# Performance work log

Hardware: AMD Instinct MI355X
Metric: run time of the kernel (lower is better)

The kernel has to match this reference:

```python
import jax, jax.numpy as jnp
import numpy as np

N_NODES = 100000
N_EDGES = 3200000
N_FEAT = 256
N_CLASS = 40
K_HOPS = 2


def setup_inputs() -> dict:
    key = jax.random.key(0)
    k1, k2, k3, k4, k5 = jax.random.split(key, 5)
    x = jax.random.normal(k1, (N_NODES, N_FEAT), dtype=jnp.float32)
    edge_index = jax.random.randint(k2, (2, N_EDGES), 0, N_NODES, dtype=jnp.int64)
    edge_weight = jax.random.uniform(k3, (N_EDGES,), dtype=jnp.float32)
    W = jax.random.normal(k4, (N_CLASS, N_FEAT), dtype=jnp.float32) / np.sqrt(N_FEAT)
    b = jax.random.normal(k5, (N_CLASS,), dtype=jnp.float32) * 0.01
    return {"x": x, "edge_index": edge_index, "edge_weight": edge_weight, "W": W, "b": b}


def _sgc_forward(x, edge_index, edge_weight, W, b):
    n = x.shape[0]
    # gcn_norm with add_self_loops=True (SGConv default, fill_value=1.0)
    self_idx = jnp.arange(n, dtype=edge_index.dtype)
    row = jnp.concatenate([edge_index[0], self_idx])
    col = jnp.concatenate([edge_index[1], self_idx])
    w = jnp.concatenate([edge_weight, jnp.ones((n,), dtype=edge_weight.dtype)])
    deg = jax.ops.segment_sum(w, col, num_segments=n)  # degree at targets
    dinv = jnp.where(deg > 0, jax.lax.rsqrt(deg), 0.0)
    norm = dinv[row] * w * dinv[col]  # [E+N]
    # K-hop propagation: out[col] += norm * x[row]
    for _ in range(K_HOPS):
        x = jax.ops.segment_sum(norm[:, None] * x[row], col, num_segments=n)
    logits = x @ W.T + b  # [N, nclass]
    return jax.nn.log_softmax(logits, axis=1)


def reference(x, edge_index, edge_weight, W, b):
    return _sgc_forward(x, edge_index, edge_weight, W, b)
```

## Files before the change

kernel.cpp:

```cpp
#include <hip/hip_runtime.h>
#include <hip/hip_fp16.h>
#include <cmath>

#define NNODES 100000
#define NEDGES 3200000
#define NFEAT 256
#define NCLASS 40

#define BSHIFT 8
#define BSIZE 256
#define NBUCK ((NNODES + BSIZE - 1) / BSIZE)
#define CAP 9216
#define ECHUNK 8192
#define CSTH 512
#define EPT (ECHUNK / CSTH)
#define NCB ((NEDGES + ECHUNK - 1) / ECHUNK)
#define EPTF (CAP / 512)


using bf16x8 = __attribute__((ext_vector_type(8))) short;
using f32x4 = __attribute__((ext_vector_type(4))) float;

__device__ inline unsigned pk2(float a, float b) {
    __half2 h;
    h.x = __float2half_rn(a);
    h.y = __float2half_rn(b);
    return *reinterpret_cast<unsigned*>(&h);
}
__device__ inline float2 up2(unsigned u) {
    __half2 h = *reinterpret_cast<__half2*>(&u);
    float2 f;
    f.x = __half2float(h.x);
    f.y = __half2float(h.y);
    return f;
}
__device__ inline unsigned short f2bf(float f) {
    unsigned u = __float_as_uint(f);
    unsigned r = (u + 0x7FFFu + ((u >> 16) & 1u)) >> 16;
    return (unsigned short)r;
}

__global__ void detect_kernel(const int* __restrict__ eidx, int* __restrict__ flag) {
    __shared__ int odd_nz;
    if (threadIdx.x == 0) odd_nz = 0;
    __syncthreads();
    int local = 0;
    for (int i = threadIdx.x; i < 2048; i += blockDim.x) {
        if (eidx[2 * i + 1] != 0) local = 1;
    }
    if (local) atomicOr(&odd_nz, 1);
    __syncthreads();
    if (threadIdx.x == 0) *flag = odd_nz ? 1 : 2;
}

__global__ void __launch_bounds__(CSTH) cscatter_kernel(const int* __restrict__ eidx,
                                                        const float* __restrict__ ew,
                                                        int2* __restrict__ coarse,
                                                        int* __restrict__ cursor,
                                                        const int* __restrict__ flag) {
    __shared__ int h[NBUCK];
    __shared__ int lbase[NBUCK];
    int t = threadIdx.x;
    for (int i = t; i < NBUCK; i += CSTH) h[i] = 0;
    __syncthreads();
    int stride = *flag;
    long long cb = (long long)NEDGES * stride;
    int e0 = blockIdx.x * ECHUNK;
    int bk[EPT];
    int pk[EPT];
    float wv[EPT];
#pragma unroll
    for (int i = 0; i < EPT; i++) {
        int e = e0 + t + i * CSTH;
        if (e < NEDGES) {
            int col = eidx[cb + (long long)e * stride];
            int src = eidx[(long long)e * stride];
            wv[i] = ew[e];
            bk[i] = col >> BSHIFT;
            pk[i] = (src << BSHIFT) | (col & (BSIZE - 1));
            atomicAdd(&h[bk[i]], 1);
        } else {
            bk[i] = -1;
        }
    }
    __syncthreads();
    for (int i = t; i < NBUCK; i += CSTH) {
        int c = h[i];
        lbase[i] = c ? atomicAdd(&cursor[i], c) : 0;
        h[i] = 0;
    }
    __syncthreads();
#pragma unroll
    for (int i = 0; i < EPT; i++) {
        if (bk[i] >= 0) {
            int pos = lbase[bk[i]] + atomicAdd(&h[bk[i]], 1);
            coarse[(size_t)bk[i] * CAP + pos] = make_int2(pk[i], __float_as_int(wv[i]));
        }
    }
}

__global__ void __launch_bounds__(512) fine_kernel(int2* __restrict__ coarse,
                                                   const int* __restrict__ cursor,
                                                   int* __restrict__ rowptr,
                                                   int* __restrict__ rowend,
                                                   float* __restrict__ dinv,
                                                   const int* __restrict__ unused) {
    __shared__ int hist[BSIZE];
    __shared__ float wdeg[BSIZE];
    __shared__ int foff[BSIZE];
    __shared__ int sa[BSIZE], sb[BSIZE];
    int t = threadIdx.x;
    int bk = blockIdx.x;
    size_t base = (size_t)bk * CAP;
    if (t < BSIZE) { hist[t] = 0; wdeg[t] = 0.f; }
    __syncthreads();
    int cnt = cursor[bk];
    int2 st[EPTF];
#pragma unroll
    for (int i = 0; i < EPTF; i++) {
        int idx = t + i * 512;
        if (idx < cnt) st[i] = coarse[base + idx];
    }
#pragma unroll
    for (int i = 0; i < EPTF; i++) {
        int idx = t + i * 512;
        if (idx < cnt) {
            int loc = st[i].x & (BSIZE - 1);
            atomicAdd(&hist[loc], 1);
            atomicAdd(&wdeg[loc], __int_as_float(st[i].y));
        }
    }
    __syncthreads();
    int gcol = (bk << BSHIFT) + t;
    if (t < BSIZE) {
        float dv = rsqrtf(wdeg[t] + 1.0f);
        if (gcol < NNODES) dinv[gcol] = dv;
        sa[t] = hist[t];
    }
    __syncthreads();
    int* s = sa; int* d = sb;
    for (int off = 1; off < BSIZE; off <<= 1) {
        if (t < BSIZE) d[t] = s[t] + ((t >= off) ? s[t - off] : 0);
        __syncthreads();
        int* tmp = s; s = d; d = tmp;
    }
    if (t < BSIZE) {
        foff[t] = (t == 0) ? 0 : s[t - 1];
        hist[t] = 0;
        if (gcol < NNODES) {
            rowptr[gcol] = (int)base + foff[t];
            rowend[gcol] = (int)base + s[t];
        }
    }
    __syncthreads();
#pragma unroll
    for (int i = 0; i < EPTF; i++) {
        int idx = t + i * 512;
        if (idx < cnt) {
            int loc = st[i].x & (BSIZE - 1);
            int srcn = ((unsigned)st[i].x) >> BSHIFT;
            int pos = foff[loc] + atomicAdd(&hist[loc], 1);
            coarse[base + pos] = make_int2(srcn, st[i].y);
        }
    }
}

__global__ void wconv_kernel(const float* __restrict__ W, unsigned short* __restrict__ wt) {
    int i = blockIdx.x * 256 + threadIdx.x;
    if (i >= 48 * 256) return;
    int n = i >> 8;
    wt[i] = (n < NCLASS) ? f2bf(W[i]) : (unsigned short)0;
}

__global__ void __launch_bounds__(256) gemm_mfma_kernel(const float* __restrict__ x,
                                                        const unsigned short* __restrict__ wt,
                                                        const float* __restrict__ dinv,
                                                        __half* __restrict__ y0h) {
    int wv = threadIdx.x >> 6;
    int lane = threadIdx.x & 63;
    int r = lane & 15;
    int kg = lane >> 4;
    int mbase = blockIdx.x * 64 + wv * 16;
    int anode = mbase + r;
    bool aok = anode < NNODES;
    const float* ap = x + (size_t)anode * NFEAT + kg * 8;

    f32x4 acc0 = {0.f, 0.f, 0.f, 0.f};
    f32x4 acc1 = {0.f, 0.f, 0.f, 0.f};
    f32x4 acc2 = {0.f, 0.f, 0.f, 0.f};
#pragma unroll
    for (int ks = 0; ks < 8; ks++) {
        int k0 = ks * 32 + kg * 8;
        bf16x8 af;
        if (aok) {
            float4 p0 = *(const float4*)(ap + ks * 32);
            float4 p1 = *(const float4*)(ap + ks * 32 + 4);
            af[0] = (short)f2bf(p0.x); af[1] = (short)f2bf(p0.y);
            af[2] = (short)f2bf(p0.z); af[3] = (short)f2bf(p0.w);
            af[4] = (short)f2bf(p1.x); af[5] = (short)f2bf(p1.y);
            af[6] = (short)f2bf(p1.z); af[7] = (short)f2bf(p1.w);
        } else {
            af = bf16x8{0, 0, 0, 0, 0, 0, 0, 0};
        }
        bf16x8 b0 = *(const bf16x8*)(wt + (0 * 16 + r) * NFEAT + k0);
        bf16x8 b1 = *(const bf16x8*)(wt + (1 * 16 + r) * NFEAT + k0);
        bf16x8 b2 = *(const bf16x8*)(wt + (2 * 16 + r) * NFEAT + k0);
        acc0 = __builtin_amdgcn_mfma_f32_16x16x32_bf16(af, b0, acc0, 0, 0, 0);
        acc1 = __builtin_amdgcn_mfma_f32_16x16x32_bf16(af, b1, acc1, 0, 0, 0);
        acc2 = __builtin_amdgcn_mfma_f32_16x16x32_bf16(af, b2, acc2, 0, 0, 0);
    }
#pragma unroll
    for (int j = 0; j < 4; j++) {
        int node = mbase + kg * 4 + j;
        if (node >= NNODES) continue;
        float dv = dinv[node];
        __half* yr = y0h + (size_t)node * 64;
        yr[r] = __float2half_rn(acc0[j] * dv);
        yr[16 + r] = __float2half_rn(acc1[j] * dv);
        if (r < 8) yr[32 + r] = __float2half_rn(acc2[j] * dv);
    }
}

__global__ void __launch_bounds__(320) hop16_kernel(const int* __restrict__ rowptr,
                                                    const int* __restrict__ rowend,
                                                    const int2* __restrict__ csr,
                                                    const float* __restrict__ dinv,
                                                    const uint4* __restrict__ yin,
                                                    uint4* __restrict__ yout) {
    int tid = threadIdx.x;
    int ln = tid / 5;
    int c = tid - ln * 5;
    int n = blockIdx.x * 64 + ln;
    if (n >= NNODES) return;
    float d = dinv[n];
    float dd = d * d;
    uint4 sv = yin[(size_t)n * 8 + c];
    float a0, a1, a2, a3, a4, a5, a6, a7;
    { float2 u0 = up2(sv.x), u1 = up2(sv.y), u2 = up2(sv.z), u3 = up2(sv.w);
      a0 = u0.x; a1 = u0.y; a2 = u1.x; a3 = u1.y; a4 = u2.x; a5 = u2.y; a6 = u3.x; a7 = u3.y; }
    int e0 = rowptr[n], e1 = rowend[n];
    int e = e0;
    for (; e + 8 <= e1; e += 8) {
        int2 p[8];
        uint4 g[8];
#pragma unroll
        for (int i = 0; i < 8; i++) p[i] = csr[e + i];
#pragma unroll
        for (int i = 0; i < 8; i++) g[i] = yin[(size_t)p[i].x * 8 + c];
#pragma unroll
        for (int i = 0; i < 8; i++) {
            float w = __int_as_float(p[i].y);
            float2 u0 = up2(g[i].x), u1 = up2(g[i].y), u2 = up2(g[i].z), u3 = up2(g[i].w);
            a0 += w * u0.x; a1 += w * u0.y; a2 += w * u1.x; a3 += w * u1.y;
            a4 += w * u2.x; a5 += w * u2.y; a6 += w * u3.x; a7 += w * u3.y;
        }
    }
    for (; e < e1; e++) {
        int2 p = csr[e];
        uint4 g = yin[(size_t)p.x * 8 + c];
        float w = __int_as_float(p.y);
        float2 u0 = up2(g.x), u1 = up2(g.y), u2 = up2(g.z), u3 = up2(g.w);
        a0 += w * u0.x; a1 += w * u0.y; a2 += w * u1.x; a3 += w * u1.y;
        a4 += w * u2.x; a5 += w * u2.y; a6 += w * u3.x; a7 += w * u3.y;
    }
    uint4 o;
    o.x = pk2(dd * a0, dd * a1); o.y = pk2(dd * a2, dd * a3);
    o.z = pk2(dd * a4, dd * a5); o.w = pk2(dd * a6, dd * a7);
    yout[(size_t)n * 8 + c] = o;
}

__global__ void __launch_bounds__(320) hop32_kernel(const int* __restrict__ rowptr,
                                                    const int* __restrict__ rowend,
                                                    const int2* __restrict__ csr,
                                                    const float* __restrict__ dinv,
                                                    const uint4* __restrict__ yin,
                                                    const float* __restrict__ bias,
                                                    float* __restrict__ out) {
    __shared__ float redm[64][5];
    __shared__ float reds[64][5];
    int tid = threadIdx.x;
    int ln = tid / 5;
    int c = tid - ln * 5;
    int n = blockIdx.x * 64 + ln;
    bool alive = n < NNODES;
    float d = alive ? dinv[n] : 0.f;
    float a0 = 0, a1 = 0, a2 = 0, a3 = 0, a4 = 0, a5 = 0, a6 = 0, a7 = 0;
    int e0 = 0, e1 = 0;
    if (alive) {
        uint4 sv = yin[(size_t)n * 8 + c];
        float2 u0 = up2(sv.x), u1 = up2(sv.y), u2 = up2(sv.z), u3 = up2(sv.w);
        a0 = u0.x; a1 = u0.y; a2 = u1.x; a3 = u1.y; a4 = u2.x; a5 = u2.y; a6 = u3.x; a7 = u3.y;
        e0 = rowptr[n]; e1 = rowend[n];
    }
    int e = e0;
    for (; e + 8 <= e1; e += 8) {
        int2 p[8];
        uint4 g[8];
#pragma unroll
        for (int i = 0; i < 8; i++) p[i] = csr[e + i];
#pragma unroll
        for (int i = 0; i < 8; i++) g[i] = yin[(size_t)p[i].x * 8 + c];
#pragma unroll
        for (int i = 0; i < 8; i++) {
            float w = __int_as_float(p[i].y);
            float2 u0 = up2(g[i].x), u1 = up2(g[i].y), u2 = up2(g[i].z), u3 = up2(g[i].w);
            a0 += w * u0.x; a1 += w * u0.y; a2 += w * u1.x; a3 += w * u1.y;
            a4 += w * u2.x; a5 += w * u2.y; a6 += w * u3.x; a7 += w * u3.y;
        }
    }
    for (; e < e1; e++) {
        int2 p = csr[e];
        uint4 g = yin[(size_t)p.x * 8 + c];
        float w = __int_as_float(p.y);
        float2 u0 = up2(g.x), u1 = up2(g.y), u2 = up2(g.z), u3 = up2(g.w);
        a0 += w * u0.x; a1 += w * u0.y; a2 += w * u1.x; a3 += w * u1.y;
        a4 += w * u2.x; a5 += w * u2.y; a6 += w * u3.x; a7 += w * u3.y;
    }
    float4 b0 = *(const float4*)(bias + c * 8);
    float4 b1 = *(const float4*)(bias + c * 8 + 4);
    float v0 = d * a0 + b0.x, v1 = d * a1 + b0.y, v2 = d * a2 + b0.z, v3 = d * a3 + b0.w;
    float v4 = d * a4 + b1.x, v5 = d * a5 + b1.y, v6 = d * a6 + b1.z, v7 = d * a7 + b1.w;
    float mm = fmaxf(fmaxf(fmaxf(v0, v1), fmaxf(v2, v3)), fmaxf(fmaxf(v4, v5), fmaxf(v6, v7)));
    redm[ln][c] = mm;
    __syncthreads();
    if (c == 0) {
        float m = redm[ln][0];
#pragma unroll
        for (int j = 1; j < 5; j++) m = fmaxf(m, redm[ln][j]);
        redm[ln][0] = m;
    }
    __syncthreads();
    float m = redm[ln][0];
    float ss = __expf(v0 - m) + __expf(v1 - m) + __expf(v2 - m) + __expf(v3 - m)
             + __expf(v4 - m) + __expf(v5 - m) + __expf(v6 - m) + __expf(v7 - m);
    reds[ln][c] = ss;
    __syncthreads();
    if (c == 0) {
        float s = 0.f;
#pragma unroll
        for (int j = 0; j < 5; j++) s += reds[ln][j];
        reds[ln][0] = logf(s);
    }
    __syncthreads();
    float ls = reds[ln][0];
    if (alive) {
        float* op = out + (size_t)n * NCLASS + c * 8;
        *(float4*)op = make_float4(v0 - m - ls, v1 - m - ls, v2 - m - ls, v3 - m - ls);
        *(float4*)(op + 4) = make_float4(v4 - m - ls, v5 - m - ls, v6 - m - ls, v7 - m - ls);
    }
}

extern "C" void kernel_launch(void* const* d_in, const int* in_sizes, int n_in,
                              void* d_out, int out_size, void* d_ws, size_t ws_size,
                              hipStream_t stream) {
    const float* x = (const float*)d_in[0];
    const int* eidx = (const int*)d_in[1];
    const float* ew = (const float*)d_in[2];
    const float* W = (const float*)d_in[3];
    const float* b = (const float*)d_in[4];
    float* out = (float*)d_out;

    char* ws = (char*)d_ws;
    size_t off = 0;
    auto alloc = [&](size_t bytes) -> char* {
        char* p = ws + off;
        off += (bytes + 255) & ~(size_t)255;
        return p;
    };
    int* flag = (int*)alloc(sizeof(int));
    int* cursor = (int*)alloc((size_t)NBUCK * 4);
    int* rowptr = (int*)alloc((size_t)NNODES * 4);
    int* rowend = (int*)alloc((size_t)NNODES * 4);
    float* dinv = (float*)alloc((size_t)NNODES * 4);
    unsigned short* wt = (unsigned short*)alloc((size_t)48 * 256 * 2);
    int2* gcsr = (int2*)alloc((size_t)NBUCK * CAP * 8);
    __half* y0h = (__half*)alloc((size_t)NNODES * 128);
    __half* y1h = (__half*)alloc((size_t)NNODES * 128);

    hipMemsetAsync(cursor, 0, (size_t)NBUCK * 4, stream);
    detect_kernel<<<1, 256, 0, stream>>>(eidx, flag);
    wconv_kernel<<<48, 256, 0, stream>>>(W, wt);
    cscatter_kernel<<<NCB, CSTH, 0, stream>>>(eidx, ew, gcsr, cursor, flag);
    fine_kernel<<<NBUCK, 512, 0, stream>>>(gcsr, cursor, rowptr, rowend, dinv, flag);
    gemm_mfma_kernel<<<(NNODES + 63) / 64, 256, 0, stream>>>(x, wt, dinv, y0h);
    hop16_kernel<<<(NNODES + 63) / 64, 320, 0, stream>>>(rowptr, rowend, gcsr, dinv,
                                                         (const uint4*)y0h, (uint4*)y1h);
    hop32_kernel<<<(NNODES + 63) / 64, 320, 0, stream>>>(rowptr, rowend, gcsr, dinv,
                                                         (const uint4*)y1h, b, out);
}
```

Before: 248.9 us.

## Split propagation into column slabs and pack CSR entries into 32 bits

Splits the 40-class feature matrix into three narrow slabs (16, 16, 8 columns) that are each propagated through both hops separately, so each slab's gather working set is smaller and more cache-resident. CSR entries are packed into 32 bits (17-bit source index plus a 15-bit half-precision weight), halving index traffic, and row start and end are merged into one int2. Log-softmax moves to a separate wave-reduction kernel that re-reads the logits. The cost is three times the CSR traversals, more launches, an extra pass over the output, and reduced weight precision.

```diff
diff --git a/kernel.cpp b/kernel.cpp
--- a/kernel.cpp
+++ b/kernel.cpp
@@ -101,10 +101,8 @@
 
 __global__ void __launch_bounds__(512) fine_kernel(int2* __restrict__ coarse,
                                                    const int* __restrict__ cursor,
-                                                   int* __restrict__ rowptr,
-                                                   int* __restrict__ rowend,
-                                                   float* __restrict__ dinv,
-                                                   const int* __restrict__ unused) {
+                                                   int2* __restrict__ rowmeta,
+                                                   float* __restrict__ dinv) {
     __shared__ int hist[BSIZE];
     __shared__ float wdeg[BSIZE];
     __shared__ int foff[BSIZE];
@@ -112,6 +110,8 @@
     int t = threadIdx.x;
     int bk = blockIdx.x;
     size_t base = (size_t)bk * CAP;
+    unsigned* csr32 = (unsigned*)coarse;
+    int base2 = bk * CAP * 2;
     if (t < BSIZE) { hist[t] = 0; wdeg[t] = 0.f; }
     __syncthreads();
     int cnt = cursor[bk];
@@ -147,10 +147,7 @@
     if (t < BSIZE) {
         foff[t] = (t == 0) ? 0 : s[t - 1];
         hist[t] = 0;
-        if (gcol < NNODES) {
-            rowptr[gcol] = (int)base + foff[t];
-            rowend[gcol] = (int)base + s[t];
-        }
+        if (gcol < NNODES) rowmeta[gcol] = make_int2(base2 + foff[t], base2 + s[t]);
     }
     __syncthreads();
 #pragma unroll
@@ -158,9 +155,10 @@
         int idx = t + i * 512;
         if (idx < cnt) {
             int loc = st[i].x & (BSIZE - 1);
-            int srcn = ((unsigned)st[i].x) >> BSHIFT;
+            unsigned srcn = ((unsigned)st[i].x) >> BSHIFT;
             int pos = foff[loc] + atomicAdd(&hist[loc], 1);
-            coarse[base + pos] = make_int2(srcn, st[i].y);
+            unsigned wb = (unsigned)__half_as_ushort(__float2half_rn(__int_as_float(st[i].y))) & 0x7FFFu;
+            csr32[base2 + pos] = (srcn << 15) | wb;
         }
     }
 }
@@ -175,7 +173,9 @@
 __global__ void __launch_bounds__(256) gemm_mfma_kernel(const float* __restrict__ x,
                                                         const unsigned short* __restrict__ wt,
                                                         const float* __restrict__ dinv,
-                                                        __half* __restrict__ y0h) {
+                                                        __half* __restrict__ S0,
+                                                        __half* __restrict__ S1,
+                                                        __half* __restrict__ S2) {
     int wv = threadIdx.x >> 6;
     int lane = threadIdx.x & 63;
     int r = lane & 15;
@@ -214,51 +214,49 @@
         int node = mbase + kg * 4 + j;
         if (node >= NNODES) continue;
         float dv = dinv[node];
-        __half* yr = y0h + (size_t)node * 64;
-        yr[r] = __float2half_rn(acc0[j] * dv);
-        yr[16 + r] = __float2half_rn(acc1[j] * dv);
-        if (r < 8) yr[32 + r] = __float2half_rn(acc2[j] * dv);
-    }
-}
-
-__global__ void __launch_bounds__(320) hop16_kernel(const int* __restrict__ rowptr,
-                                                    const int* __restrict__ rowend,
-                                                    const int2* __restrict__ csr,
-                                                    const float* __restrict__ dinv,
-                                                    const uint4* __restrict__ yin,
-                                                    uint4* __restrict__ yout) {
-    int tid = threadIdx.x;
-    int ln = tid / 5;
-    int c = tid - ln * 5;
-    int n = blockIdx.x * 64 + ln;
+        S0[(size_t)node * 16 + r] = __float2half_rn(acc0[j] * dv);
+        S1[(size_t)node * 16 + r] = __float2half_rn(acc1[j] * dv);
+        if (r < 8) S2[(size_t)node * 8 + r] = __float2half_rn(acc2[j] * dv);
+    }
+}
+
+template <int LPN>
+__global__ void __launch_bounds__(320) hopA_kernel(const int2* __restrict__ rowmeta,
+                                                   const unsigned* __restrict__ csr,
+                                                   const float* __restrict__ dinv,
+                                                   const uint4* __restrict__ yin,
+                                                   uint4* __restrict__ yout) {
+    int idx = blockIdx.x * blockDim.x + threadIdx.x;
+    int n = idx / LPN;
+    int half = idx - n * LPN;
     if (n >= NNODES) return;
     float d = dinv[n];
     float dd = d * d;
-    uint4 sv = yin[(size_t)n * 8 + c];
+    int2 rm = rowmeta[n];
+    uint4 sv = yin[(size_t)n * LPN + half];
     float a0, a1, a2, a3, a4, a5, a6, a7;
     { float2 u0 = up2(sv.x), u1 = up2(sv.y), u2 = up2(sv.z), u3 = up2(sv.w);
       a0 = u0.x; a1 = u0.y; a2 = u1.x; a3 = u1.y; a4 = u2.x; a5 = u2.y; a6 = u3.x; a7 = u3.y; }
-    int e0 = rowptr[n], e1 = rowend[n];
-    int e = e0;
+    int e = rm.x, e1 = rm.y;
     for (; e + 8 <= e1; e += 8) {
-        int2 p[8];
+        unsigned p[8];
         uint4 g[8];
 #pragma unroll
         for (int i = 0; i < 8; i++) p[i] = csr[e + i];
 #pragma unroll
-        for (int i = 0; i < 8; i++) g[i] = yin[(size_t)p[i].x * 8 + c];
+        for (int i = 0; i < 8; i++) g[i] = yin[(size_t)(p[i] >> 15) * LPN + half];
 #pragma unroll
         for (int i = 0; i < 8; i++) {
-            float w = __int_as_float(p[i].y);
+            float w = __half2float(__ushort_as_half((unsigned short)(p[i] & 0x7FFFu)));
             float2 u0 = up2(g[i].x), u1 = up2(g[i].y), u2 = up2(g[i].z), u3 = up2(g[i].w);
             a0 += w * u0.x; a1 += w * u0.y; a2 += w * u1.x; a3 += w * u1.y;
             a4 += w * u2.x; a5 += w * u2.y; a6 += w * u3.x; a7 += w * u3.y;
         }
     }
     for (; e < e1; e++) {
-        int2 p = csr[e];
-        uint4 g = yin[(size_t)p.x * 8 + c];
-        float w = __int_as_float(p.y);
+        unsigned p = csr[e];
+        uint4 g = yin[(size_t)(p >> 15) * LPN + half];
+        float w = __half2float(__ushort_as_half((unsigned short)(p & 0x7FFFu)));
         float2 u0 = up2(g.x), u1 = up2(g.y), u2 = up2(g.z), u3 = up2(g.w);
         a0 += w * u0.x; a1 += w * u0.y; a2 += w * u1.x; a3 += w * u1.y;
         a4 += w * u2.x; a5 += w * u2.y; a6 += w * u3.x; a7 += w * u3.y;
@@ -266,88 +264,73 @@
     uint4 o;
     o.x = pk2(dd * a0, dd * a1); o.y = pk2(dd * a2, dd * a3);
     o.z = pk2(dd * a4, dd * a5); o.w = pk2(dd * a6, dd * a7);
-    yout[(size_t)n * 8 + c] = o;
-}
-
-__global__ void __launch_bounds__(320) hop32_kernel(const int* __restrict__ rowptr,
-                                                    const int* __restrict__ rowend,
-                                                    const int2* __restrict__ csr,
-                                                    const float* __restrict__ dinv,
-                                                    const uint4* __restrict__ yin,
-                                                    const float* __restrict__ bias,
-                                                    float* __restrict__ out) {
-    __shared__ float redm[64][5];
-    __shared__ float reds[64][5];
-    int tid = threadIdx.x;
-    int ln = tid / 5;
-    int c = tid - ln * 5;
-    int n = blockIdx.x * 64 + ln;
-    bool alive = n < NNODES;
-    float d = alive ? dinv[n] : 0.f;
-    float a0 = 0, a1 = 0, a2 = 0, a3 = 0, a4 = 0, a5 = 0, a6 = 0, a7 = 0;
-    int e0 = 0, e1 = 0;
-    if (alive) {
-        uint4 sv = yin[(size_t)n * 8 + c];
-        float2 u0 = up2(sv.x), u1 = up2(sv.y), u2 = up2(sv.z), u3 = up2(sv.w);
-        a0 = u0.x; a1 = u0.y; a2 = u1.x; a3 = u1.y; a4 = u2.x; a5 = u2.y; a6 = u3.x; a7 = u3.y;
-        e0 = rowptr[n]; e1 = rowend[n];
-    }
-    int e = e0;
+    yout[(size_t)n * LPN + half] = o;
+}
+
+template <int LPN>
+__global__ void __launch_bounds__(320) hopB_kernel(const int2* __restrict__ rowmeta,
+                                                   const unsigned* __restrict__ csr,
+                                                   const float* __restrict__ dinv,
+                                                   const uint4* __restrict__ yin,
+                                                   const float* __restrict__ bias,
+                                                   float* __restrict__ out, int cb) {
+    int idx = blockIdx.x * blockDim.x + threadIdx.x;
+    int n = idx / LPN;
+    int half = idx - n * LPN;
+    if (n >= NNODES) return;
+    float d = dinv[n];
+    int2 rm = rowmeta[n];
+    uint4 sv = yin[(size_t)n * LPN + half];
+    float a0, a1, a2, a3, a4, a5, a6, a7;
+    { float2 u0 = up2(sv.x), u1 = up2(sv.y), u2 = up2(sv.z), u3 = up2(sv.w);
+      a0 = u0.x; a1 = u0.y; a2 = u1.x; a3 = u1.y; a4 = u2.x; a5 = u2.y; a6 = u3.x; a7 = u3.y; }
+    int e = rm.x, e1 = rm.y;
     for (; e + 8 <= e1; e += 8) {
-        int2 p[8];
+        unsigned p[8];
         uint4 g[8];
 #pragma unroll
         for (int i = 0; i < 8; i++) p[i] = csr[e + i];
 #pragma unroll
-        for (int i = 0; i < 8; i++) g[i] = yin[(size_t)p[i].x * 8 + c];
+        for (int i = 0; i < 8; i++) g[i] = yin[(size_t)(p[i] >> 15) * LPN + half];
 #pragma unroll
         for (int i = 0; i < 8; i++) {
-            float w = __int_as_float(p[i].y);
+            float w = __half2float(__ushort_as_half((unsigned short)(p[i] & 0x7FFFu)));
             float2 u0 = up2(g[i].x), u1 = up2(g[i].y), u2 = up2(g[i].z), u3 = up2(g[i].w);
             a0 += w * u0.x; a1 += w * u0.y; a2 += w * u1.x; a3 += w * u1.y;
             a4 += w * u2.x; a5 += w * u2.y; a6 += w * u3.x; a7 += w * u3.y;
         }
     }
     for (; e < e1; e++) {
-        int2 p = csr[e];
-        uint4 g = yin[(size_t)p.x * 8 + c];
-        float w = __int_as_float(p.y);
+        unsigned p = csr[e];
+        uint4 g = yin[(size_t)(p >> 15) * LPN + half];
+        float w = __half2float(__ushort_as_half((unsigned short)(p & 0x7FFFu)));
         float2 u0 = up2(g.x), u1 = up2(g.y), u2 = up2(g.z), u3 = up2(g.w);
         a0 += w * u0.x; a1 += w * u0.y; a2 += w * u1.x; a3 += w * u1.y;
         a4 += w * u2.x; a5 += w * u2.y; a6 += w * u3.x; a7 += w * u3.y;
     }
-    float4 b0 = *(const float4*)(bias + c * 8);
-    float4 b1 = *(const float4*)(bias + c * 8 + 4);
-    float v0 = d * a0 + b0.x, v1 = d * a1 + b0.y, v2 = d * a2 + b0.z, v3 = d * a3 + b0.w;
-    float v4 = d * a4 + b1.x, v5 = d * a5 + b1.y, v6 = d * a6 + b1.z, v7 = d * a7 + b1.w;
-    float mm = fmaxf(fmaxf(fmaxf(v0, v1), fmaxf(v2, v3)), fmaxf(fmaxf(v4, v5), fmaxf(v6, v7)));
-    redm[ln][c] = mm;
-    __syncthreads();
-    if (c == 0) {
-        float m = redm[ln][0];
-#pragma unroll
-        for (int j = 1; j < 5; j++) m = fmaxf(m, redm[ln][j]);
-        redm[ln][0] = m;
-    }
-    __syncthreads();
-    float m = redm[ln][0];
-    float ss = __expf(v0 - m) + __expf(v1 - m) + __expf(v2 - m) + __expf(v3 - m)
-             + __expf(v4 - m) + __expf(v5 - m) + __expf(v6 - m) + __expf(v7 - m);
-    reds[ln][c] = ss;
-    __syncthreads();
-    if (c == 0) {
-        float s = 0.f;
-#pragma unroll
-        for (int j = 0; j < 5; j++) s += reds[ln][j];
-        reds[ln][0] = logf(s);
-    }
-    __syncthreads();
-    float ls = reds[ln][0];
-    if (alive) {
-        float* op = out + (size_t)n * NCLASS + c * 8;
-        *(float4*)op = make_float4(v0 - m - ls, v1 - m - ls, v2 - m - ls, v3 - m - ls);
-        *(float4*)(op + 4) = make_float4(v4 - m - ls, v5 - m - ls, v6 - m - ls, v7 - m - ls);
-    }
+    const float* bp = bias + cb + half * 8;
+    float4 b0 = *(const float4*)bp;
+    float4 b1 = *(const float4*)(bp + 4);
+    float* op = out + (size_t)n * NCLASS + cb + half * 8;
+    *(float4*)op = make_float4(d * a0 + b0.x, d * a1 + b0.y, d * a2 + b0.z, d * a3 + b0.w);
+    *(float4*)(op + 4) = make_float4(d * a4 + b1.x, d * a5 + b1.y, d * a6 + b1.z, d * a7 + b1.w);
+}
+
+__global__ void softmax_kernel(float* __restrict__ out) {
+    int gtid = blockIdx.x * blockDim.x + threadIdx.x;
+    int wid = gtid >> 6;
+    int lane = threadIdx.x & 63;
+    if (wid >= NNODES) return;
+    float* r = out + (size_t)wid * NCLASS;
+    float v = (lane < NCLASS) ? r[lane] : -INFINITY;
+    float m = v;
+#pragma unroll
+    for (int o = 32; o; o >>= 1) m = fmaxf(m, __shfl_xor(m, o));
+    float e = (lane < NCLASS) ? __expf(v - m) : 0.f;
+    float s = e;
+#pragma unroll
+    for (int o = 32; o; o >>= 1) s += __shfl_xor(s, o);
+    if (lane < NCLASS) r[lane] = v - m - logf(s);
 }
 
 extern "C" void kernel_launch(void* const* d_in, const int* in_sizes, int n_in,
@@ -369,22 +352,32 @@
     };
     int* flag = (int*)alloc(sizeof(int));
     int* cursor = (int*)alloc((size_t)NBUCK * 4);
-    int* rowptr = (int*)alloc((size_t)NNODES * 4);
-    int* rowend = (int*)alloc((size_t)NNODES * 4);
+    int2* rowmeta = (int2*)alloc((size_t)NNODES * 8);
     float* dinv = (float*)alloc((size_t)NNODES * 4);
     unsigned short* wt = (unsigned short*)alloc((size_t)48 * 256 * 2);
     int2* gcsr = (int2*)alloc((size_t)NBUCK * CAP * 8);
-    __half* y0h = (__half*)alloc((size_t)NNODES * 128);
-    __half* y1h = (__half*)alloc((size_t)NNODES * 128);
+    __half* S0a = (__half*)alloc((size_t)NNODES * 32);
+    __half* S1a = (__half*)alloc((size_t)NNODES * 32);
+    __half* S2a = (__half*)alloc((size_t)NNODES * 16);
+    __half* S0b = (__half*)alloc((size_t)NNODES * 32);
+    __half* S1b = (__half*)alloc((size_t)NNODES * 32);
+    __half* S2b = (__half*)alloc((size_t)NNODES * 16);
 
     hipMemsetAsync(cursor, 0, (size_t)NBUCK * 4, stream);
     detect_kernel<<<1, 256, 0, stream>>>(eidx, flag);
     wconv_kernel<<<48, 256, 0, stream>>>(W, wt);
     cscatter_kernel<<<NCB, CSTH, 0, stream>>>(eidx, ew, gcsr, cursor, flag);
-    fine_kernel<<<NBUCK, 512, 0, stream>>>(gcsr, cursor, rowptr, rowend, dinv, flag);
-    gemm_mfma_kernel<<<(NNODES + 63) / 64, 256, 0, stream>>>(x, wt, dinv, y0h);
-    hop16_kernel<<<(NNODES + 63) / 64, 320, 0, stream>>>(rowptr, rowend, gcsr, dinv,
-                                                         (const uint4*)y0h, (uint4*)y1h);
-    hop32_kernel<<<(NNODES + 63) / 64, 320, 0, stream>>>(rowptr, rowend, gcsr, dinv,
-                                                         (const uint4*)y1h, b, out);
-}
+    fine_kernel<<<NBUCK, 512, 0, stream>>>(gcsr, cursor, rowmeta, dinv);
+    gemm_mfma_kernel<<<(NNODES + 63) / 64, 256, 0, stream>>>(x, wt, dinv, S0a, S1a, S2a);
+
+    const unsigned* csr = (const unsigned*)gcsr;
+    int g2 = (NNODES * 2 + 319) / 320;
+    int g1 = (NNODES + 255) / 256;
+    hopA_kernel<2><<<g2, 320, 0, stream>>>(rowmeta, csr, dinv, (const uint4*)S0a, (uint4*)S0b);
+    hopB_kernel<2><<<g2, 320, 0, stream>>>(rowmeta, csr, dinv, (const uint4*)S0b, b, out, 0);
+    hopA_kernel<2><<<g2, 320, 0, stream>>>(rowmeta, csr, dinv, (const uint4*)S1a, (uint4*)S1b);
+    hopB_kernel<2><<<g2, 320, 0, stream>>>(rowmeta, csr, dinv, (const uint4*)S1b, b, out, 16);
+    hopA_kernel<1><<<g1, 256, 0, stream>>>(rowmeta, csr, dinv, (const uint4*)S2a, (uint4*)S2b);
+    hopB_kernel<1><<<g1, 256, 0, stream>>>(rowmeta, csr, dinv, (const uint4*)S2b, b, out, 32);
+    softmax_kernel<<<(NNODES + 3) / 4, 256, 0, stream>>>(out);
+}
```

Result: slower. 300.2 us (+20.6%).
